# Optimization experiments

Measured on AMD Instinct MI355X. Metric: run time of the kernel, lower is better.

Reference implementation:

```python
import jax, jax.numpy as jnp
import numpy as np

WS = 7            # window_size (attention is over 7x7x1 windows)
DIM = 128
DIM_HEAD = 32
HEADS = DIM // DIM_HEAD
SCALE = DIM_HEAD ** -0.5


def _rel_pos_indices(ws):
    # matches torch: 2D meshgrid over window_size, flattened, pairwise diffs
    pos = np.arange(ws)
    gi, gj = np.meshgrid(pos, pos, indexing='ij')
    grid = np.stack([gi.reshape(-1), gj.reshape(-1)], axis=-1)          # (ws^2, 2)
    rel = grid[:, None, :] - grid[None, :, :] + (ws - 1)                # (ws^2, ws^2, 2)
    idx = rel[..., 0] * (2 * ws - 1) + rel[..., 1]                      # (ws^2, ws^2)
    return jnp.asarray(idx, dtype=jnp.int32)


def setup_inputs() -> dict:
    key = jax.random.key(0)
    k1, k2, k3, k4 = jax.random.split(key, 4)
    x = jax.random.normal(k1, (4, 16, 16, 8, WS, WS, 1, DIM), dtype=jnp.float32)
    w_qkv = jax.random.normal(k2, (DIM, 3 * DIM), dtype=jnp.float32) * 0.02
    w_out = jax.random.normal(k3, (DIM, DIM), dtype=jnp.float32) * 0.02
    bias_table = jax.random.normal(k4, ((2 * WS - 1) ** 2, HEADS), dtype=jnp.float32) * 0.02
    return {"x": x, "w_qkv": w_qkv, "w_out": w_out, "bias_table": bias_table}


def reference(x, w_qkv, w_out, bias_table):
    b, X, Y, Z, w1, w2, w3, d = x.shape
    h, dh = HEADS, DIM_HEAD
    n = w1 * w2 * w3                                  # 49 tokens per window
    B = b * X * Y * Z                                 # fused window batch
    xf = x.reshape(B, n, d)
    qkv = xf @ w_qkv                                  # (B, n, 3d), no bias
    q, k, v = jnp.split(qkv, 3, axis=-1)

    def to_heads(t):
        return t.reshape(B, n, h, dh).transpose(0, 2, 1, 3)   # (B, h, n, dh)

    q = to_heads(q) * SCALE
    k = to_heads(k)
    v = to_heads(v)

    sim = jnp.einsum('bhid,bhjd->bhij', q, k)          # (B, h, n, n)
    bias = bias_table[_rel_pos_indices(WS)]            # (n, n, h) gather
    sim = sim + bias.transpose(2, 0, 1)                # broadcast over B
    attn = jax.nn.softmax(sim, axis=-1)                # dropout p=0.0
    out = jnp.einsum('bhij,bhjd->bhid', attn, v)       # (B, h, n, dh)
    out = out.transpose(0, 2, 1, 3).reshape(B, w1, w2, w3, d)
    out = out @ w_out                                  # (B, w1, w2, w3, d)
    return out.reshape(b, X, Y, Z, w1, w2, w3, d)
```

## Files before the change

kernel.cpp:

```cpp
#include <hip/hip_runtime.h>


typedef __bf16 bf16x8 __attribute__((ext_vector_type(8)));
typedef float f32x4 __attribute__((ext_vector_type(4)));
typedef unsigned short u16x8 __attribute__((ext_vector_type(8)));

__device__ __forceinline__ unsigned short bf16c(float f) {
  return __builtin_bit_cast(unsigned short, (__bf16)f);
}
__device__ __forceinline__ bf16x8 ld8(const unsigned short* p) {
  return __builtin_bit_cast(bf16x8, *(const u16x8*)p);
}

__global__ void prep(const float* __restrict__ wq, const float* __restrict__ wo,
                     const float* __restrict__ bt,
                     unsigned short* __restrict__ wTq,
                     unsigned short* __restrict__ wTo,
                     float* __restrict__ bias2) {
  int t = blockIdx.x * 256 + threadIdx.x;
  if (t < 49152) {
    int n = t >> 7, k = t & 127;
    float v = wq[k * 384 + n];
    if (n < 128) v *= 0.17677669529663689f;
    wTq[t] = bf16c(v);
  } else if (t < 65536) {
    int i = t - 49152;
    int n = i >> 7, k = i & 127;
    wTo[i] = bf16c(wo[k * 128 + n]);
  } else {
    int i = t - 65536;
    int r = i & 3, q = (i >> 2) & 3, jt = (i >> 4) & 3;
    int c = (i >> 6) & 15, it = (i >> 10) & 3, h = (i >> 12) & 3;
    int j = jt * 16 + q * 4 + r;
    int ii = it * 16 + c;
    int iq = ii < 49 ? ii : 48;
    float v = -1e30f;
    if (j < 49) {
      int ri = iq / 7 - j / 7 + 6;
      int rj = iq % 7 - j % 7 + 6;
      v = bt[(ri * 13 + rj) * 4 + h];
    }
    bias2[i] = v;
  }
}

__global__ __launch_bounds__(256, 3) void attn_fused(
    const float* __restrict__ x,
    const unsigned short* __restrict__ wTq,
    const unsigned short* __restrict__ wTo,
    const f32x4* __restrict__ bias2,
    float* __restrict__ out) {
  __shared__ __align__(16) unsigned short lds[8192];

  const int tid = threadIdx.x;
  const int wave = tid >> 6;
  const int lane = tid & 63;
  const int c16 = lane & 15;
  const int quad = lane >> 4;
  const int q4 = quad * 4;
  const int h = wave;
  const f32x4 zero4 = {0.f, 0.f, 0.f, 0.f};

  const float* xb = x + (size_t)blockIdx.x * 6272;

  for (int c = tid; c < 1024; c += 256) {
    int row = c >> 4, c8 = c & 15;
    bf16x8 v;
    if (row < 49) {
      const float4* p = (const float4*)(xb + row * 128 + c8 * 8);
      float4 f0 = p[0], f1 = p[1];
      v[0] = (__bf16)f0.x; v[1] = (__bf16)f0.y; v[2] = (__bf16)f0.z; v[3] = (__bf16)f0.w;
      v[4] = (__bf16)f1.x; v[5] = (__bf16)f1.y; v[6] = (__bf16)f1.z; v[7] = (__bf16)f1.w;
    } else {
#pragma unroll
      for (int e = 0; e < 8; ++e) v[e] = (__bf16)0.f;
    }
    *(u16x8*)&lds[row * 128 + ((c8 ^ (row & 7)) << 3)] = __builtin_bit_cast(u16x8, v);
  }
  __syncthreads();

  const u16x8* wq8 = (const u16x8*)wTq;
  bf16x8 bq[4];
  bf16x8 ak[4];
  bf16x8 bv[2][2];

#pragma unroll
  for (int p = 0; p < 2; ++p) {
    f32x4 acc[4][2];
#pragma unroll
    for (int m = 0; m < 4; ++m) { acc[m][0] = zero4; acc[m][1] = zero4; }
#pragma unroll
    for (int kk = 0; kk < 4; ++kk) {
      bf16x8 a[4];
#pragma unroll
      for (int m = 0; m < 4; ++m)
        a[m] = ld8(&lds[(16 * m + c16) * 128 + ((((kk << 2) | quad) ^ (c16 & 7)) << 3)]);
#pragma unroll
      for (int j = 0; j < 2; ++j) {
        bf16x8 b = __builtin_bit_cast(bf16x8,
                   wq8[(p * 128 + h * 32 + j * 16 + c16) * 16 + (kk << 2) + quad]);
#pragma unroll
        for (int m = 0; m < 4; ++m)
          acc[m][j] = __builtin_amdgcn_mfma_f32_16x16x32_bf16(b, a[m], acc[m][j], 0, 0, 0);
      }
    }
    if (p == 0) {
#pragma unroll
      for (int it = 0; it < 4; ++it)
#pragma unroll
        for (int e = 0; e < 8; ++e)
          bq[it][e] = (__bf16)acc[it][e >> 2][e & 3];
    } else {
#pragma unroll
      for (int jt = 0; jt < 4; ++jt)
#pragma unroll
        for (int e = 0; e < 8; ++e)
          ak[jt][e] = (__bf16)acc[jt][e >> 2][e & 3];
    }
  }
#pragma unroll
  for (int j2 = 0; j2 < 2; ++j2) {
    f32x4 acc2[4];
#pragma unroll
    for (int m = 0; m < 4; ++m) acc2[m] = zero4;
#pragma unroll
    for (int kk = 0; kk < 4; ++kk) {
      bf16x8 b = __builtin_bit_cast(bf16x8,
                 wq8[(256 + h * 32 + j2 * 16 + c16) * 16 + (kk << 2) + quad]);
#pragma unroll
      for (int m = 0; m < 4; ++m) {
        bf16x8 a = ld8(&lds[(16 * m + c16) * 128 + ((((kk << 2) | quad) ^ (c16 & 7)) << 3)]);
        acc2[m] = __builtin_amdgcn_mfma_f32_16x16x32_bf16(a, b, acc2[m], 0, 0, 0);
      }
    }
#pragma unroll
    for (int m = 0; m < 4; ++m)
#pragma unroll
      for (int r = 0; r < 4; ++r)
        bv[m >> 1][j2][4 * (m & 1) + r] = (__bf16)acc2[m][r];
  }
  __syncthreads();

#pragma unroll
  for (int it = 0; it < 4; ++it) {
    f32x4 s[4];
#pragma unroll
    for (int jt = 0; jt < 4; ++jt) {
      f32x4 b4 = bias2[((h * 4 + it) * 16 + c16) * 16 + jt * 4 + quad];
      s[jt] = __builtin_amdgcn_mfma_f32_16x16x32_bf16(ak[jt], bq[it], b4, 0, 0, 0);
    }
    float e[4][4];
#pragma unroll
    for (int jt = 0; jt < 4; ++jt)
#pragma unroll
      for (int r = 0; r < 4; ++r)
        e[jt][r] = __expf(s[jt][r]);
    float rs = ((e[0][0] + e[0][1]) + (e[0][2] + e[0][3]))
             + ((e[1][0] + e[1][1]) + (e[1][2] + e[1][3]))
             + ((e[2][0] + e[2][1]) + (e[2][2] + e[2][3]))
             + ((e[3][0] + e[3][1]) + (e[3][2] + e[3][3]));
    rs += __shfl_xor(rs, 16);
    rs += __shfl_xor(rs, 32);
    float rinv = __builtin_amdgcn_rcpf(rs);
    bf16x8 pa[2];
#pragma unroll
    for (int kk = 0; kk < 2; ++kk)
#pragma unroll
      for (int ee = 0; ee < 8; ++ee)
        pa[kk][ee] = (__bf16)(e[2 * kk + (ee >> 2)][ee & 3] * rinv);
    f32x4 o0 = zero4, o1 = zero4;
#pragma unroll
    for (int kk = 0; kk < 2; ++kk) {
      o0 = __builtin_amdgcn_mfma_f32_16x16x32_bf16(pa[kk], bv[kk][0], o0, 0, 0, 0);
      o1 = __builtin_amdgcn_mfma_f32_16x16x32_bf16(pa[kk], bv[kk][1], o1, 0, 0, 0);
    }
#pragma unroll
    for (int r = 0; r < 4; ++r) {
      int row = 16 * it + q4 + r;
      if (row < 49) {
        lds[row * 136 + h * 32 + c16]      = bf16c(o0[r]);
        lds[row * 136 + h * 32 + 16 + c16] = bf16c(o1[r]);
      }
    }
  }
  __syncthreads();

  const u16x8* wo8 = (const u16x8*)wTo;
  const int MOFF2[4] = {0, 16, 32, 33};
  f32x4 oc[4][2];
#pragma unroll
  for (int m = 0; m < 4; ++m) { oc[m][0] = zero4; oc[m][1] = zero4; }
#pragma unroll
  for (int kk = 0; kk < 4; ++kk) {
    bf16x8 a2[4];
#pragma unroll
    for (int m = 0; m < 4; ++m)
      a2[m] = ld8(&lds[(MOFF2[m] + c16) * 136 + kk * 32 + quad * 8]);
#pragma unroll
    for (int j = 0; j < 2; ++j) {
      bf16x8 b2 = __builtin_bit_cast(bf16x8,
                  wo8[((2 * wave + j) * 16 + c16) * 16 + (kk << 2) + quad]);
#pragma unroll
      for (int m = 0; m < 4; ++m)
        oc[m][j] = __builtin_amdgcn_mfma_f32_16x16x32_bf16(a2[m], b2, oc[m][j], 0, 0, 0);
    }
  }

  float* op = out + (size_t)blockIdx.x * 6272;
#pragma unroll
  for (int m = 0; m < 4; ++m)
#pragma unroll
    for (int r = 0; r < 4; ++r) {
      int row = MOFF2[m] + q4 + r;
      if (m == 3 && row != 48) continue;
#pragma unroll
      for (int j = 0; j < 2; ++j)
        op[row * 128 + (2 * wave + j) * 16 + c16] = oc[m][j][r];
    }
}

extern "C" void kernel_launch(void* const* d_in, const int* in_sizes, int n_in,
                              void* d_out, int out_size, void* d_ws, size_t ws_size,
                              hipStream_t stream) {
  const float* x = (const float*)d_in[0];
  const float* wq = (const float*)d_in[1];
  const float* wo = (const float*)d_in[2];
  const float* bt = (const float*)d_in[3];

  unsigned short* wTq = (unsigned short*)d_ws;
  unsigned short* wTo = wTq + 49152;
  float* bias2 = (float*)((char*)d_ws + 131072);

  prep<<<320, 256, 0, stream>>>(wq, wo, bt, wTq, wTo, bias2);
  attn_fused<<<8192, 256, 0, stream>>>(x, wTq, wTo, (const f32x4*)bias2, (float*)d_out);
}
```

Baseline: 497.6 us.

## Defer softmax normalization to PV output, raise occupancy bound, nontemporal stores

Raises the launch-bounds minimum blocks per CU from 3 to 5, forcing the compiler to cap registers for more resident waves. The softmax loop is restructured so exponentials are converted to bf16 right after each score MFMA, without keeping a full 16-float array live. The 1/rowsum scaling moves to after the PV MFMA, fetched per output row with a shuffle. Output stores become nontemporal to avoid polluting cache. Risks register spills under the tighter bound, plus slightly different rounding from normalizing after the bf16 cast.

```diff
diff --git a/kernel.cpp b/kernel.cpp
--- a/kernel.cpp
+++ b/kernel.cpp
@@ -44,7 +44,7 @@
   }
 }
 
-__global__ __launch_bounds__(256, 3) void attn_fused(
+__global__ __launch_bounds__(256, 5) void attn_fused(
     const float* __restrict__ x,
     const unsigned short* __restrict__ wTq,
     const unsigned short* __restrict__ wTo,
@@ -143,31 +143,25 @@
 
 #pragma unroll
   for (int it = 0; it < 4; ++it) {
-    f32x4 s[4];
+    bf16x8 pa[2];
+    float rs = 0.f;
 #pragma unroll
     for (int jt = 0; jt < 4; ++jt) {
       f32x4 b4 = bias2[((h * 4 + it) * 16 + c16) * 16 + jt * 4 + quad];
-      s[jt] = __builtin_amdgcn_mfma_f32_16x16x32_bf16(ak[jt], bq[it], b4, 0, 0, 0);
-    }
-    float e[4][4];
-#pragma unroll
-    for (int jt = 0; jt < 4; ++jt)
-#pragma unroll
-      for (int r = 0; r < 4; ++r)
-        e[jt][r] = __expf(s[jt][r]);
-    float rs = ((e[0][0] + e[0][1]) + (e[0][2] + e[0][3]))
-             + ((e[1][0] + e[1][1]) + (e[1][2] + e[1][3]))
-             + ((e[2][0] + e[2][1]) + (e[2][2] + e[2][3]))
-             + ((e[3][0] + e[3][1]) + (e[3][2] + e[3][3]));
+      f32x4 s = __builtin_amdgcn_mfma_f32_16x16x32_bf16(ak[jt], bq[it], b4, 0, 0, 0);
+      float e0 = __expf(s[0]);
+      float e1 = __expf(s[1]);
+      float e2 = __expf(s[2]);
+      float e3 = __expf(s[3]);
+      rs += (e0 + e1) + (e2 + e3);
+      pa[jt >> 1][(jt & 1) * 4 + 0] = (__bf16)e0;
+      pa[jt >> 1][(jt & 1) * 4 + 1] = (__bf16)e1;
+      pa[jt >> 1][(jt & 1) * 4 + 2] = (__bf16)e2;
+      pa[jt >> 1][(jt & 1) * 4 + 3] = (__bf16)e3;
+    }
     rs += __shfl_xor(rs, 16);
     rs += __shfl_xor(rs, 32);
     float rinv = __builtin_amdgcn_rcpf(rs);
-    bf16x8 pa[2];
-#pragma unroll
-    for (int kk = 0; kk < 2; ++kk)
-#pragma unroll
-      for (int ee = 0; ee < 8; ++ee)
-        pa[kk][ee] = (__bf16)(e[2 * kk + (ee >> 2)][ee & 3] * rinv);
     f32x4 o0 = zero4, o1 = zero4;
 #pragma unroll
     for (int kk = 0; kk < 2; ++kk) {
@@ -176,10 +170,11 @@
     }
 #pragma unroll
     for (int r = 0; r < 4; ++r) {
+      float rf = __shfl(rinv, (lane & 48) | (q4 + r));
       int row = 16 * it + q4 + r;
       if (row < 49) {
-        lds[row * 136 + h * 32 + c16]      = bf16c(o0[r]);
-        lds[row * 136 + h * 32 + 16 + c16] = bf16c(o1[r]);
+        lds[row * 136 + h * 32 + c16]      = bf16c(o0[r] * rf);
+        lds[row * 136 + h * 32 + 16 + c16] = bf16c(o1[r] * rf);
       }
     }
   }
@@ -215,7 +210,8 @@
       if (m == 3 && row != 48) continue;
 #pragma unroll
       for (int j = 0; j < 2; ++j)
-        op[row * 128 + (2 * wave + j) * 16 + c16] = oc[m][j][r];
+        __builtin_nontemporal_store(oc[m][j][r],
+            &op[row * 128 + (2 * wave + j) * 16 + c16]);
     }
 }
 
```

New measurement: 718.5 us. +44.4%, slower.
